# Performance work log

Hardware: AMD Instinct MI355X
Metric: run time of the kernel (lower is better)

Reference implementation:

```python
import jax, jax.numpy as jnp
import numpy as np

EPS = 1e-5
NUM_HEADS = 4
HEAD_DIM = 64
NUM_STEPS = 3


def layernorm(x, g, b):
    mu = jnp.mean(x, axis=-1, keepdims=True)
    var = jnp.mean((x - mu) ** 2, axis=-1, keepdims=True)
    return (x - mu) / jnp.sqrt(var + EPS) * g + b


def entmax15(x):
    # exact alpha=1.5 entmax along last axis (Peters et al. 2019)
    n = x.shape[-1]
    x = x - jnp.max(x, axis=-1, keepdims=True)
    x = x / 2.0
    srt = -jnp.sort(-x, axis=-1)                      # descending
    rho = jnp.arange(1, n + 1, dtype=x.dtype)
    cs = jnp.cumsum(srt, axis=-1)
    cs2 = jnp.cumsum(srt * srt, axis=-1)
    mean = cs / rho
    ss = cs2 - mean * cs                              # k * (mean_sq - mean^2)
    delta = (1.0 - ss) / rho
    d = jnp.clip(delta, 0.0)
    safe = jnp.where(d > 0, d, 1.0)
    tau = mean - jnp.where(d > 0, jnp.sqrt(safe), 0.0)
    support = (tau <= srt).astype(jnp.int32)
    k_star = jnp.sum(support, axis=-1, keepdims=True) - 1
    tau_star = jnp.take_along_axis(tau, k_star, axis=-1)
    p = jnp.clip(x - tau_star, 0.0)
    return p * p


def setup_inputs() -> dict:
    key = jax.random.key(0)
    ks = jax.random.split(key, 8)
    B, S, Dh = 2, 512, 2048
    N, Dm = 8192, 1024
    T = NUM_HEADS * HEAD_DIM  # 256
    hidden = jax.random.normal(ks[0], (B, S, Dh), dtype=jnp.float32)
    memory = jax.random.normal(ks[1], (N, Dm), dtype=jnp.float32)
    Wq = jax.random.normal(ks[2], (Dh, T), dtype=jnp.float32) * 0.02
    Wk = jax.random.normal(ks[3], (Dm, T), dtype=jnp.float32) * 0.02
    Wv = jax.random.normal(ks[4], (Dm, T), dtype=jnp.float32) * 0.02
    Wo = jax.random.normal(ks[5], (T, Dh), dtype=jnp.float32) * 0.02
    log_beta = jnp.full((NUM_HEADS,), float(np.log(1.0 / np.sqrt(HEAD_DIM))), dtype=jnp.float32)
    g_s = jnp.ones((Dh,), jnp.float32)
    b_s = jnp.zeros((Dh,), jnp.float32)
    g_m = jnp.ones((Dm,), jnp.float32)
    b_m = jnp.zeros((Dm,), jnp.float32)
    return {"hidden": hidden, "memory": memory, "Wq": Wq, "Wk": Wk, "Wv": Wv,
            "Wo": Wo, "log_beta": log_beta, "g_s": g_s, "b_s": b_s,
            "g_m": g_m, "b_m": b_m}


def reference(hidden, memory, Wq, Wk, Wv, Wo, log_beta, g_s, b_s, g_m, b_m):
    B, S, _ = hidden.shape
    N = memory.shape[0]
    H, D = NUM_HEADS, HEAD_DIM
    Q = layernorm(hidden, g_s, b_s) @ Wq                         # [B,S,H*D]
    mem_n = layernorm(memory, g_m, b_m)
    K = (mem_n @ Wk).reshape(N, H, D).transpose(1, 0, 2)         # [H,N,D]
    V = (mem_n @ Wv).reshape(N, H, D).transpose(1, 0, 2)         # [H,N,D]
    xi = Q.reshape(B, S, H, D).transpose(0, 2, 1, 3)             # [B,H,S,D]
    beta = jnp.exp(log_beta)[None, :, None, None]                # [1,H,1,1]
    for _ in range(NUM_STEPS):
        scores = jnp.einsum('bhsd,hnd->bhsn', xi, K) * beta      # [B,H,S,N]
        w = entmax15(scores)
        xi = jnp.einsum('bhsn,hnd->bhsd', w, V)
    converged = xi.transpose(0, 2, 1, 3).reshape(B, S, H * D)
    output = converged @ Wo                                      # [B,S,hidden_dim]
    return output, converged
```

## Files before the change

### kernel.cpp

```cpp
#include <hip/hip_runtime.h>
#include <math.h>

typedef _Float16 f16;
typedef f16 f16x8 __attribute__((ext_vector_type(8)));
typedef float f32x4 __attribute__((ext_vector_type(4)));

#define QSCALE 16384.0f
#define QINV 6.103515625e-5f
#define QOFF 2.5f

__device__ __forceinline__ float wred_add(float v) {
#pragma unroll
  for (int off = 32; off >= 1; off >>= 1) v += __shfl_xor(v, off, 64);
  return v;
}
__device__ __forceinline__ float wred_max(float v) {
#pragma unroll
  for (int off = 32; off >= 1; off >>= 1) v = fmaxf(v, __shfl_xor(v, off, 64));
  return v;
}

__global__ __launch_bounds__(256) void ln_stats_all_kernel(
    const float* __restrict__ hidden, const float* __restrict__ memory,
    float* __restrict__ mu_h, float* __restrict__ rs_h,
    float* __restrict__ mu_m, float* __restrict__ rs_m) {
  int b = blockIdx.x, tid = threadIdx.x;
  const float* X;
  float* mu;
  float* rs;
  int cols, row;
  if (b < 1024) { X = hidden; cols = 2048; mu = mu_h; rs = rs_h; row = b; }
  else { X = memory; cols = 1024; mu = mu_m; rs = rs_m; row = b - 1024; }
  const float4* xr = (const float4*)(X + (size_t)row * cols);
  int nv = cols >> 10;
  float s = 0.f, s2 = 0.f;
  for (int v = 0; v < nv; ++v) {
    float4 x4 = xr[tid + (v << 8)];
    s += x4.x + x4.y + x4.z + x4.w;
    s2 += x4.x * x4.x + x4.y * x4.y + x4.z * x4.z + x4.w * x4.w;
  }
  s = wred_add(s);
  s2 = wred_add(s2);
  __shared__ float rb[8];
  int wid = tid >> 6, lane = tid & 63;
  if (lane == 0) { rb[wid] = s; rb[4 + wid] = s2; }
  __syncthreads();
  if (tid == 0) {
    float S = rb[0] + rb[1] + rb[2] + rb[3];
    float S2 = rb[4] + rb[5] + rb[6] + rb[7];
    float m = S / (float)cols;
    float var = S2 / (float)cols - m * m;
    mu[row] = m;
    rs[row] = 1.f / sqrtf(var + 1e-5f);
  }
}

__global__ __launch_bounds__(256) void split_a_all_kernel(
    const float* __restrict__ hidden, const float* __restrict__ memory,
    const float* __restrict__ mu_h, const float* __restrict__ rs_h,
    const float* __restrict__ mu_m, const float* __restrict__ rs_m,
    f16x8* __restrict__ Ahh, f16x8* __restrict__ Ahl,
    f16x8* __restrict__ Amh, f16x8* __restrict__ Aml) {
  int b = blockIdx.x;
  const float* X;
  const float* mu;
  const float* rs;
  f16x8 *Ah, *Al;
  int M, Kd, b0;
  if (b < 1024) {
    X = hidden; mu = mu_h; rs = rs_h; Ah = Ahh; Al = Ahl;
    M = 1024; Kd = 2048; b0 = 0;
  } else {
    X = memory; mu = mu_m; rs = rs_m; Ah = Amh; Al = Aml;
    M = 8192; Kd = 1024; b0 = 1024;
  }
  int blk = (b - b0) * 4 + (threadIdx.x >> 6);
  int l = threadIdx.x & 63;
  int nmt = M >> 4;
  int kc = blk / nmt, mt = blk - kc * nmt;
  int m = mt * 16 + (l & 15);
  int k = kc * 32 + ((l >> 4) << 3);
  const float* src = X + (size_t)m * Kd + k;
  float mm = mu[m];
  float rr = rs[m];
  f16x8 hi, lo;
#pragma unroll
  for (int j = 0; j < 8; ++j) {
    float v = (src[j] - mm) * rr;
    f16 hv = (f16)v;
    hi[j] = hv;
    lo[j] = (f16)((v - (float)hv) * 512.f);
  }
  size_t o = ((size_t)blk << 6) + l;
  Ah[o] = hi;
  Al[o] = lo;
}

__global__ __launch_bounds__(256) void split_a_kernel(
    const float* __restrict__ X, const float* __restrict__ mu,
    const float* __restrict__ rs, f16x8* __restrict__ Ah,
    f16x8* __restrict__ Al, int M, int Kd, int lay) {
  int blk = blockIdx.x * 4 + (threadIdx.x >> 6);
  int l = threadIdx.x & 63;
  int nmt = M >> 4;
  int kc = blk / nmt, mt = blk - kc * nmt;
  int m = mt * 16 + (l & 15);
  int k = kc * 32 + ((l >> 4) << 3);
  const float* src;
  if (lay == 0) {
    src = X + (size_t)m * Kd + k;
  } else {
    int b = m >> 9, s = m & 511, hh = k >> 6, d = k & 63;
    src = X + ((((size_t)b * 4 + hh) * 512 + s) << 6) + d;
  }
  float mm = mu ? mu[m] : 0.f;
  float rr = rs ? rs[m] : 1.f;
  f16x8 hi, lo;
#pragma unroll
  for (int j = 0; j < 8; ++j) {
    float v = (src[j] - mm) * rr;
    f16 hv = (f16)v;
    hi[j] = hv;
    lo[j] = (f16)((v - (float)hv) * 512.f);
  }
  size_t o = ((size_t)blk << 6) + l;
  Ah[o] = hi;
  Al[o] = lo;
}

__global__ __launch_bounds__(256) void split_w_all_kernel(
    const float* __restrict__ Wq, const float* __restrict__ Wk,
    const float* __restrict__ Wv, const float* __restrict__ Wo,
    const float* __restrict__ g_s, const float* __restrict__ g_m,
    f16x8* __restrict__ Bqh, f16x8* __restrict__ Bql,
    f16x8* __restrict__ Bkh, f16x8* __restrict__ Bkl,
    f16x8* __restrict__ Bvh, f16x8* __restrict__ Bvl,
    f16x8* __restrict__ Boh, f16x8* __restrict__ Bol) {
  int b = blockIdx.x;
  const float* W;
  const float* g;
  f16x8 *Bh, *Bl;
  int N, base;
  if (b < 256) { W = Wq; g = g_s; Bh = Bqh; Bl = Bql; N = 256; base = 0; }
  else if (b < 384) { W = Wk; g = g_m; Bh = Bkh; Bl = Bkl; N = 256; base = 256; }
  else if (b < 512) { W = Wv; g = g_m; Bh = Bvh; Bl = Bvl; N = 256; base = 384; }
  else { W = Wo; g = nullptr; Bh = Boh; Bl = Bol; N = 2048; base = 512; }
  int blk = (b - base) * 4 + (threadIdx.x >> 6);
  int l = threadIdx.x & 63;
  int nnt = N >> 4;
  int kc = blk / nnt, nt = blk - kc * nnt;
  int n = nt * 16 + (l & 15);
  int k0 = kc * 32 + ((l >> 4) << 3);
  f16x8 hi, lo;
#pragma unroll
  for (int j = 0; j < 8; ++j) {
    float v = W[(size_t)(k0 + j) * N + n];
    if (g) v *= g[k0 + j];
    f16 hv = (f16)v;
    hi[j] = hv;
    lo[j] = (f16)((v - (float)hv) * 512.f);
  }
  size_t o = ((size_t)blk << 6) + l;
  Bh[o] = hi;
  Bl[o] = lo;
}

__global__ __launch_bounds__(256) void wcol3_kernel(
    const float* __restrict__ Wq, const float* __restrict__ bq,
    const float* __restrict__ Wk, const float* __restrict__ bk,
    const float* __restrict__ Wv, const float* __restrict__ bv,
    float* __restrict__ vbq, float* __restrict__ vbk,
    float* __restrict__ vbv) {
  int which = blockIdx.z;
  const float* W = which == 0 ? Wq : (which == 1 ? Wk : Wv);
  const float* b = which == 0 ? bq : (which == 1 ? bk : bv);
  float* vb = which == 0 ? vbq : (which == 1 ? vbk : vbv);
  int Kd = which == 0 ? 2048 : 1024;
  int t = threadIdx.x;
  int kpb = Kd >> 4;
  int k0 = blockIdx.y * kpb;
  float s = 0.f;
  for (int k = k0; k < k0 + kpb; ++k) s = fmaf(b[k], W[(size_t)k * 256 + t], s);
  atomicAdd(&vb[t], s);
}

__global__ __launch_bounds__(256) void gemm_mfma_kernel(
    const f16x8* __restrict__ Ah, const f16x8* __restrict__ Al,
    const f16x8* __restrict__ Bh, const f16x8* __restrict__ Bl,
    const float* __restrict__ vb, float* __restrict__ outf,
    f16x8* __restrict__ o16a, f16x8* __restrict__ o16b, int M, int N, int nk,
    int out_mode) {
  __shared__ __align__(16) float Ts[64][68];
  const int tid = threadIdx.x;
  const int w = tid >> 6, l = tid & 63;
  const int ql = l & 15, g = l >> 4;
  const int bn = blockIdx.x, bm = blockIdx.y;
  const size_t astr = ((size_t)(M >> 4)) << 6;
  const size_t bstr = ((size_t)(N >> 4)) << 6;
  const f16x8* aph = Ah + (((size_t)(bm * 4 + w)) << 6) + l;
  const f16x8* apl = Al + (((size_t)(bm * 4 + w)) << 6) + l;
  const f16x8* bph = Bh + (((size_t)(bn * 4)) << 6) + l;
  const f16x8* bpl = Bl + (((size_t)(bn * 4)) << 6) + l;

  f32x4 cm[4], cx[4];
#pragma unroll
  for (int nf = 0; nf < 4; ++nf) {
    cm[nf] = (f32x4){0.f, 0.f, 0.f, 0.f};
    cx[nf] = (f32x4){0.f, 0.f, 0.f, 0.f};
  }

  f16x8 a0h = aph[0], a0l = apl[0];
  f16x8 b0h[4], b0l[4];
#pragma unroll
  for (int nf = 0; nf < 4; ++nf) {
    b0h[nf] = bph[nf << 6];
    b0l[nf] = bpl[nf << 6];
  }

  for (int kc = 0; kc < nk - 1; ++kc) {
    const size_t ao = (size_t)(kc + 1) * astr;
    const size_t bo = (size_t)(kc + 1) * bstr;
    f16x8 a1h = aph[ao], a1l = apl[ao];
    f16x8 b1h[4], b1l[4];
#pragma unroll
    for (int nf = 0; nf < 4; ++nf) {
      b1h[nf] = bph[bo + (nf << 6)];
      b1l[nf] = bpl[bo + (nf << 6)];
    }
#pragma unroll
    for (int nf = 0; nf < 4; ++nf) {
      cm[nf] = __builtin_amdgcn_mfma_f32_16x16x32_f16(a0h, b0h[nf], cm[nf], 0, 0, 0);
      cx[nf] = __builtin_amdgcn_mfma_f32_16x16x32_f16(a0h, b0l[nf], cx[nf], 0, 0, 0);
      cx[nf] = __builtin_amdgcn_mfma_f32_16x16x32_f16(a0l, b0h[nf], cx[nf], 0, 0, 0);
    }
    a0h = a1h;
    a0l = a1l;
#pragma unroll
    for (int nf = 0; nf < 4; ++nf) {
      b0h[nf] = b1h[nf];
      b0l[nf] = b1l[nf];
    }
  }
#pragma unroll
  for (int nf = 0; nf < 4; ++nf) {
    cm[nf] = __builtin_amdgcn_mfma_f32_16x16x32_f16(a0h, b0h[nf], cm[nf], 0, 0, 0);
    cx[nf] = __builtin_amdgcn_mfma_f32_16x16x32_f16(a0h, b0l[nf], cx[nf], 0, 0, 0);
    cx[nf] = __builtin_amdgcn_mfma_f32_16x16x32_f16(a0l, b0h[nf], cx[nf], 0, 0, 0);
  }

  float vbc[4] = {0.f, 0.f, 0.f, 0.f};
  if (vb) {
#pragma unroll
    for (int nf = 0; nf < 4; ++nf) vbc[nf] = vb[bn * 64 + nf * 16 + ql];
  }

  if (out_mode == 0) {
#pragma unroll
    for (int nf = 0; nf < 4; ++nf)
#pragma unroll
      for (int r = 0; r < 4; ++r) {
        float val = fmaf(cx[nf][r], 0.001953125f, cm[nf][r]) + vbc[nf];
        int m = bm * 64 + w * 16 + (g << 2) + r;
        int n = bn * 64 + nf * 16 + ql;
        int b = m >> 9, s = m & 511, hh = n >> 6, d = n & 63;
        outf[((((size_t)b * 4 + hh) * 512 + s) << 6) + d] = val;
      }
  } else if (out_mode == 3) {
#pragma unroll
    for (int nf = 0; nf < 4; ++nf)
#pragma unroll
      for (int r = 0; r < 4; ++r) {
        float val = fmaf(cx[nf][r], 0.001953125f, cm[nf][r]) + vbc[nf];
        int m = bm * 64 + w * 16 + (g << 2) + r;
        int n = bn * 64 + nf * 16 + ql;
        outf[(size_t)m * N + n] = val;
      }
  } else {
#pragma unroll
    for (int nf = 0; nf < 4; ++nf)
#pragma unroll
      for (int r = 0; r < 4; ++r)
        Ts[w * 16 + (g << 2) + r][nf * 16 + ql] =
            fmaf(cx[nf][r], 0.001953125f, cm[nf][r]) + vbc[nf];
    __syncthreads();
    if (out_mode == 4) {
#pragma unroll
      for (int i = 0; i < 2; ++i) {
        int slot = tid + (i << 8);
        int blk = slot >> 6, l2 = slot & 63;
        int ktl = blk >> 1, dc = blk & 1;
        int key = (ktl << 4) + (l2 & 15);
        int db = (dc << 5) + ((l2 >> 4) << 3);
        f16x8 hi, lo;
#pragma unroll
        for (int j = 0; j < 8; ++j) {
          float v = Ts[key][db + j];
          f16 hv = (f16)v;
          hi[j] = hv;
          lo[j] = (f16)((v - (float)hv) * 512.f);
        }
        size_t o = (((size_t)(bn * 512 + bm * 4 + ktl) * 2 + dc) << 6) + l2;
        o16a[o] = hi;
        o16b[o] = lo;
      }
    } else {
#pragma unroll
      for (int i = 0; i < 2; ++i) {
        int slot = tid + (i << 8);
        int blk = slot >> 6, l2 = slot & 63;
        int dt = blk >> 1, kcl = blk & 1;
        int keyb = (kcl << 5) + ((l2 >> 4) << 3);
        int d = (dt << 4) + (l2 & 15);
        f16x8 v8;
#pragma unroll
        for (int j = 0; j < 8; ++j) v8[j] = (f16)Ts[keyb + j][d];
        size_t o = (((size_t)(bn * 4 + dt) * 256 + bm * 2 + kcl) << 6) + l2;
        o16a[o] = v8;
      }
    }
  }
}

__global__ __launch_bounds__(1024) void hop_score_kernel(
    const float* __restrict__ xi_in, const f16x8* __restrict__ Khi,
    const f16x8* __restrict__ Klo, const float* __restrict__ log_beta,
    unsigned short* __restrict__ Y) {
  __shared__ float xiq[32][64];
  __shared__ float mxb[16][32];
  __shared__ float mxs[32];
  const int tid = threadIdx.x;
  const int w = tid >> 6, l = tid & 63;
  const int ql = l & 15, g = l >> 4;
  const int bh = blockIdx.x & 7;
  const int qpair = (blockIdx.x >> 3) & 15;
  const int khalf = blockIdx.x >> 7;
  const int h = bh & 3;
  const size_t base_io = ((size_t)bh * 512 + qpair * 32) * 64;

  float beta = expf(log_beta[h]);
  for (int i = tid; i < 2048; i += 1024)
    xiq[i >> 6][i & 63] = xi_in[base_io + i] * beta;
  __syncthreads();

  f16x8 xa0, xa1, xla0, xla1;
  f16x8 xb0, xb1, xlb0, xlb1;
#pragma unroll
  for (int j = 0; j < 8; ++j) {
    float a0v = xiq[ql][(g << 3) + j];
    float a1v = xiq[ql][32 + (g << 3) + j];
    float b0v = xiq[16 + ql][(g << 3) + j];
    float b1v = xiq[16 + ql][32 + (g << 3) + j];
    f16 ha0 = (f16)a0v, ha1 = (f16)a1v, hb0 = (f16)b0v, hb1 = (f16)b1v;
    xa0[j] = ha0; xla0[j] = (f16)((a0v - (float)ha0) * 512.f);
    xa1[j] = ha1; xla1[j] = (f16)((a1v - (float)ha1) * 512.f);
    xb0[j] = hb0; xlb0[j] = (f16)((b0v - (float)hb0) * 512.f);
    xb1[j] = hb1; xlb1[j] = (f16)((b1v - (float)hb1) * 512.f);
  }

  const f16x8* kb = Khi + (size_t)h * 65536 + l;
  const f16x8* kl = Klo + (size_t)h * 65536 + l;

  {
    const int kts = w * 32;
    f16x8 sa0 = kb[(size_t)kts * 128], sa1 = kb[(size_t)kts * 128 + 64];
    f32x4 cA = {0.f, 0.f, 0.f, 0.f}, cB = {0.f, 0.f, 0.f, 0.f};
    cA = __builtin_amdgcn_mfma_f32_16x16x32_f16(sa0, xa0, cA, 0, 0, 0);
    cA = __builtin_amdgcn_mfma_f32_16x16x32_f16(sa1, xa1, cA, 0, 0, 0);
    cB = __builtin_amdgcn_mfma_f32_16x16x32_f16(sa0, xb0, cB, 0, 0, 0);
    cB = __builtin_amdgcn_mfma_f32_16x16x32_f16(sa1, xb1, cB, 0, 0, 0);
    float mA = fmaxf(fmaxf(cA[0], cA[1]), fmaxf(cA[2], cA[3]));
    float mB = fmaxf(fmaxf(cB[0], cB[1]), fmaxf(cB[2], cB[3]));
    mA = fmaxf(mA, __shfl_xor(mA, 16, 64));
    mA = fmaxf(mA, __shfl_xor(mA, 32, 64));
    mB = fmaxf(mB, __shfl_xor(mB, 16, 64));
    mB = fmaxf(mB, __shfl_xor(mB, 32, 64));
    if (l < 16) { mxb[w][ql] = mA; mxb[w][16 + ql] = mB; }
  }
  __syncthreads();
  if (tid < 32) {
    float m = mxb[0][tid];
#pragma unroll
    for (int ww = 1; ww < 16; ++ww) m = fmaxf(m, mxb[ww][tid]);
    mxs[tid] = m;
  }
  __syncthreads();
  const float qcA = QOFF * QSCALE + 0.5f - mxs[ql] * 0.5f * QSCALE;
  const float qcB = QOFF * QSCALE + 0.5f - mxs[16 + ql] * 0.5f * QSCALE;

  const size_t YbaseA = (size_t)(bh * 32 + qpair * 2) * 131072;
  const size_t YbaseB = YbaseA + 131072;
  const int kt0 = khalf * 256 + w * 16;
  for (int kt = kt0; kt < kt0 + 16; ++kt) {
    f16x8 a0 = kb[(size_t)kt * 128], a1 = kb[(size_t)kt * 128 + 64];
    f16x8 b0 = kl[(size_t)kt * 128], b1 = kl[(size_t)kt * 128 + 64];
    const size_t yoff =
        (size_t)(kt >> 1) * 512 + ql * 32 + (kt & 1) * 16 + (g << 2);
    {
      f32x4 cm = {0.f, 0.f, 0.f, 0.f}, cx = {0.f, 0.f, 0.f, 0.f};
      cm = __builtin_amdgcn_mfma_f32_16x16x32_f16(a0, xa0, cm, 0, 0, 0);
      cm = __builtin_amdgcn_mfma_f32_16x16x32_f16(a1, xa1, cm, 0, 0, 0);
      cx = __builtin_amdgcn_mfma_f32_16x16x32_f16(b0, xa0, cx, 0, 0, 0);
      cx = __builtin_amdgcn_mfma_f32_16x16x32_f16(a0, xla0, cx, 0, 0, 0);
      cx = __builtin_amdgcn_mfma_f32_16x16x32_f16(b1, xa1, cx, 0, 0, 0);
      cx = __builtin_amdgcn_mfma_f32_16x16x32_f16(a1, xla1, cx, 0, 0, 0);
      ushort4 uv;
      unsigned short* up = (unsigned short*)&uv;
#pragma unroll
      for (int r = 0; r < 4; ++r) {
        float s = fmaf(cx[r], 0.001953125f, cm[r]);
        float uq = fmaf(s, 8192.0f, qcA);
        uq = fminf(fmaxf(uq, 0.f), 65535.f);
        up[r] = (unsigned short)(int)uq;
      }
      *(ushort4*)&Y[YbaseA + yoff] = uv;
    }
    {
      f32x4 cm = {0.f, 0.f, 0.f, 0.f}, cx = {0.f, 0.f, 0.f, 0.f};
      cm = __builtin_amdgcn_mfma_f32_16x16x32_f16(a0, xb0, cm, 0, 0, 0);
      cm = __builtin_amdgcn_mfma_f32_16x16x32_f16(a1, xb1, cm, 0, 0, 0);
      cx = __builtin_amdgcn_mfma_f32_16x16x32_f16(b0, xb0, cx, 0, 0, 0);
      cx = __builtin_amdgcn_mfma_f32_16x16x32_f16(a0, xlb0, cx, 0, 0, 0);
      cx = __builtin_amdgcn_mfma_f32_16x16x32_f16(b1, xb1, cx, 0, 0, 0);
      cx = __builtin_amdgcn_mfma_f32_16x16x32_f16(a1, xlb1, cx, 0, 0, 0);
      ushort4 uv;
      unsigned short* up = (unsigned short*)&uv;
#pragma unroll
      for (int r = 0; r < 4; ++r) {
        float s = fmaf(cx[r], 0.001953125f, cm[r]);
        float uq = fmaf(s, 8192.0f, qcB);
        uq = fminf(fmaxf(uq, 0.f), 65535.f);
        up[r] = (unsigned short)(int)uq;
      }
      *(ushort4*)&Y[YbaseB + yoff] = uv;
    }
  }
}

__global__ __launch_bounds__(256) void hop_tau_kernel(
    const unsigned short* __restrict__ Y, float* __restrict__ tau) {
  const int row = blockIdx.x;
  const int bh = row >> 9, qi = row & 511;
  const int qtile = qi >> 4, ql = qi & 15;
  const size_t yb = (size_t)(bh * 32 + qtile) * 131072 + ql * 32;
  const int t = threadIdx.x;
  const uint4* p = (const uint4*)(Y + yb + (size_t)t * 512);
  float y[32];
#pragma unroll
  for (int v = 0; v < 4; ++v) {
    uint4 u = p[v];
    unsigned a[4] = {u.x, u.y, u.z, u.w};
#pragma unroll
    for (int e = 0; e < 4; ++e) {
      y[v * 8 + e * 2] = fmaf((float)(a[e] & 0xffffu), QINV, -QOFF);
      y[v * 8 + e * 2 + 1] = fmaf((float)(a[e] >> 16), QINV, -QOFF);
    }
  }
  __shared__ float redm[4];
  __shared__ float rb[5][4];
  __shared__ float rb3[3][4][3];
  const int wi = t >> 6, lane = t & 63;

  {
    float m = y[0];
#pragma unroll
    for (int i = 1; i < 32; ++i) m = fmaxf(m, y[i]);
    m = wred_max(m);
    if (lane == 0) redm[wi] = m;
  }
  __syncthreads();
  const float ymax =
      fmaxf(fmaxf(redm[0], redm[1]), fmaxf(redm[2], redm[3]));

  float lo = ymax - 1.001f, hi = ymax;
#pragma unroll 1
  for (int it = 0; it < 5; ++it) {
    float tv = 0.5f * (lo + hi);
    float f = 0.f;
#pragma unroll
    for (int i = 0; i < 32; ++i) {
      float d = fmaxf(y[i] - tv, 0.f);
      f = fmaf(d, d, f);
    }
    f = wred_add(f);
    if (lane == 0) rb[it][wi] = f;
    __syncthreads();
    float tot = rb[it][0] + rb[it][1] + rb[it][2] + rb[it][3];
    if (tot >= 1.f) lo = tv; else hi = tv;
  }

  float tc = lo;
#pragma unroll 1
  for (int it = 0; it < 3; ++it) {
    float kk = 0.f, s1 = 0.f, s2 = 0.f;
#pragma unroll
    for (int i = 0; i < 32; ++i) {
      if (y[i] > tc) { kk += 1.f; s1 += y[i]; s2 = fmaf(y[i], y[i], s2); }
    }
    kk = wred_add(kk);
    s1 = wred_add(s1);
    s2 = wred_add(s2);
    if (lane == 0) { rb3[it][wi][0] = kk; rb3[it][wi][1] = s1; rb3[it][wi][2] = s2; }
    __syncthreads();
    float K = rb3[it][0][0] + rb3[it][1][0] + rb3[it][2][0] + rb3[it][3][0];
    float S1 = rb3[it][0][1] + rb3[it][1][1] + rb3[it][2][1] + rb3[it][3][1];
    float S2 = rb3[it][0][2] + rb3[it][1][2] + rb3[it][2][2] + rb3[it][3][2];
    if (K >= 0.5f) {
      float mean = S1 / K;
      float ss = fmaf(-mean, S1, S2);
      float delta = (1.f - ss) / K;
      tc = delta > 0.f ? mean - sqrtf(delta) : mean;
    }
  }
  if (t == 0) tau[row] = tc;
}

__global__ __launch_bounds__(1024) void hop_pv_kernel(
    const unsigned short* __restrict__ Y, const f16x8* __restrict__ Vp,
    const float* __restrict__ tau, float* __restrict__ xi_out) {
  __shared__ float outp[16][16][64];
  __shared__ float taus[16];
  const int tid = threadIdx.x;
  const int w = tid >> 6, l = tid & 63;
  const int ql = l & 15, g = l >> 4;
  const int bh = blockIdx.x & 7, qtile = blockIdx.x >> 3;
  const int h = bh & 3;
  const size_t base_io = ((size_t)bh * 512 + qtile * 16) * 64;

  if (tid < 16) taus[tid] = tau[bh * 512 + qtile * 16 + tid];
  __syncthreads();
  const float t1 = taus[ql];
  const size_t Ybase = (size_t)(bh * 32 + qtile) * 131072;
  const f16x8* vb = Vp + (size_t)h * 65536 + l;

  f32x4 m2[4];
#pragma unroll
  for (int dt = 0; dt < 4; ++dt) m2[dt] = (f32x4){0.f, 0.f, 0.f, 0.f};

  for (int kc = 0; kc < 16; ++kc) {
    const int chunk = w * 16 + kc;
    uint4 uv = *(const uint4*)(Y + Ybase + (size_t)chunk * 512 + ql * 32 +
                               (g << 3));
    unsigned a[4] = {uv.x, uv.y, uv.z, uv.w};
    f16x8 a2;
#pragma unroll
    for (int e = 0; e < 4; ++e) {
      float y0 = fmaf((float)(a[e] & 0xffffu), QINV, -QOFF);
      float y1 = fmaf((float)(a[e] >> 16), QINV, -QOFF);
      float p0 = fmaxf(y0 - t1, 0.f);
      float p1 = fmaxf(y1 - t1, 0.f);
      a2[e * 2] = (f16)(p0 * p0);
      a2[e * 2 + 1] = (f16)(p1 * p1);
    }
#pragma unroll
    for (int dt = 0; dt < 4; ++dt) {
      f16x8 vf = vb[(((size_t)dt * 256 + chunk) << 6)];
      m2[dt] = __builtin_amdgcn_mfma_f32_16x16x32_f16(a2, vf, m2[dt], 0, 0, 0);
    }
  }
#pragma unroll
  for (int dt = 0; dt < 4; ++dt)
#pragma unroll
    for (int r = 0; r < 4; ++r)
      outp[w][(g << 2) + r][dt * 16 + ql] = m2[dt][r];
  __syncthreads();
  {
    float s = 0.f;
#pragma unroll
    for (int ww = 0; ww < 16; ++ww) s += outp[ww][tid >> 6][tid & 63];
    xi_out[base_io + tid] = s;
  }
}

__global__ __launch_bounds__(256) void conv_copy_kernel(
    const float* __restrict__ xi, float* __restrict__ out) {
  int o4 = blockIdx.x * 256 + threadIdx.x;
  int o = o4 << 2;
  int dd = o & 63, hq = (o >> 6) & 3, sq = (o >> 8) & 511, bq = o >> 17;
  float4 v =
      *(const float4*)&xi[((((size_t)bq << 2) + hq) * 512 + sq) * 64 + dd];
  *(float4*)&out[o] = v;
}

extern "C" void kernel_launch(void* const* d_in, const int* in_sizes, int n_in,
                              void* d_out, int out_size, void* d_ws,
                              size_t ws_size, hipStream_t stream) {
  (void)in_sizes; (void)n_in; (void)out_size; (void)ws_size;
  const float* hidden = (const float*)d_in[0];
  const float* memory = (const float*)d_in[1];
  const float* Wq = (const float*)d_in[2];
  const float* Wk = (const float*)d_in[3];
  const float* Wv = (const float*)d_in[4];
  const float* Wo = (const float*)d_in[5];
  const float* log_beta = (const float*)d_in[6];
  const float* g_s = (const float*)d_in[7];
  const float* b_s = (const float*)d_in[8];
  const float* g_m = (const float*)d_in[9];
  const float* b_m = (const float*)d_in[10];
  float* out = (float*)d_out;

  float* ws = (float*)d_ws;
  float* mu_h = ws;
  float* rs_h = ws + 1024;
  float* mu_m = ws + 2048;
  float* rs_m = ws + 10240;
  float* xiA = ws + 18432;
  float* xiB = ws + 280576;
  float* vb_q = ws + 542720;
  float* vb_k = ws + 542976;
  float* vb_v = ws + 543232;
  float* tau = ws + 543488;
  f16x8* Khi = (f16x8*)(ws + 548864);
  f16x8* Klo = Khi + 262144;
  f16x8* Vp = Klo + 262144;
  f16x8* Bqh = Vp + 262144;
  f16x8* Bql = Bqh + 65536;
  f16x8* Bkh = Bql + 65536;
  f16x8* Bkl = Bkh + 32768;
  f16x8* Bvh = Bkl + 32768;
  f16x8* Bvl = Bvh + 32768;
  f16x8* Boh = Bvl + 32768;
  f16x8* Bol = Boh + 65536;
  unsigned short* Y = (unsigned short*)(Bol + 65536);
  f16x8* Amh = (f16x8*)Y;
  f16x8* Aml = Amh + 1048576;
  f16x8* Ahh = Aml + 1048576;
  f16x8* Ahl = Ahh + 262144;
  f16x8* Axh = Ahl + 262144;
  f16x8* Axl = Axh + 32768;

  ln_stats_all_kernel<<<9216, 256, 0, stream>>>(hidden, memory, mu_h, rs_h,
                                                mu_m, rs_m);
  hipMemsetAsync(vb_q, 0, 3 * 256 * sizeof(float), stream);

  split_a_all_kernel<<<5120, 256, 0, stream>>>(hidden, memory, mu_h, rs_h,
                                               mu_m, rs_m, Ahh, Ahl, Amh, Aml);
  split_w_all_kernel<<<768, 256, 0, stream>>>(Wq, Wk, Wv, Wo, g_s, g_m, Bqh,
                                              Bql, Bkh, Bkl, Bvh, Bvl, Boh,
                                              Bol);
  wcol3_kernel<<<dim3(1, 16, 3), 256, 0, stream>>>(Wq, b_s, Wk, b_m, Wv, b_m,
                                                   vb_q, vb_k, vb_v);

  gemm_mfma_kernel<<<dim3(4, 16), 256, 0, stream>>>(
      Ahh, Ahl, Bqh, Bql, vb_q, xiA, nullptr, nullptr, 1024, 256, 64, 0);
  gemm_mfma_kernel<<<dim3(4, 128), 256, 0, stream>>>(
      Amh, Aml, Bkh, Bkl, vb_k, nullptr, Khi, Klo, 8192, 256, 32, 4);
  gemm_mfma_kernel<<<dim3(4, 128), 256, 0, stream>>>(
      Amh, Aml, Bvh, Bvl, vb_v, nullptr, Vp, nullptr, 8192, 256, 32, 5);

  float* xin = xiA;
  float* xout = xiB;
  for (int step = 0; step < 3; ++step) {
    hop_score_kernel<<<256, 1024, 0, stream>>>(xin, Khi, Klo, log_beta, Y);
    hop_tau_kernel<<<4096, 256, 0, stream>>>(Y, tau);
    hop_pv_kernel<<<256, 1024, 0, stream>>>(Y, Vp, tau, xout);
    float* t = xin; xin = xout; xout = t;
  }

  split_a_kernel<<<128, 256, 0, stream>>>(xin, nullptr, nullptr, Axh, Axl,
                                          1024, 256, 1);
  gemm_mfma_kernel<<<dim3(32, 16), 256, 0, stream>>>(
      Axh, Axl, Boh, Bol, nullptr, out, nullptr, nullptr, 1024, 2048, 8, 3);
  conv_copy_kernel<<<256, 256, 0, stream>>>(xin, out + 2097152);
}
```

Baseline: 402.2 us.

## Restructure entmax tau kernel to process a 16-row query tile per block

```diff
diff --git a/kernel.cpp b/kernel.cpp
--- a/kernel.cpp
+++ b/kernel.cpp
@@ -436,55 +436,74 @@
   }
 }
 
-__global__ __launch_bounds__(256) void hop_tau_kernel(
+__global__ __launch_bounds__(1024) void hop_tau_kernel(
     const unsigned short* __restrict__ Y, float* __restrict__ tau) {
-  const int row = blockIdx.x;
-  const int bh = row >> 9, qi = row & 511;
-  const int qtile = qi >> 4, ql = qi & 15;
-  const size_t yb = (size_t)(bh * 32 + qtile) * 131072 + ql * 32;
+  const int b = blockIdx.x;
+  const size_t sb = (size_t)b * 131072;
   const int t = threadIdx.x;
-  const uint4* p = (const uint4*)(Y + yb + (size_t)t * 512);
-  float y[32];
-#pragma unroll
-  for (int v = 0; v < 4; ++v) {
-    uint4 u = p[v];
-    unsigned a[4] = {u.x, u.y, u.z, u.w};
-#pragma unroll
-    for (int e = 0; e < 4; ++e) {
-      y[v * 8 + e * 2] = fmaf((float)(a[e] & 0xffffu), QINV, -QOFF);
-      y[v * 8 + e * 2 + 1] = fmaf((float)(a[e] >> 16), QINV, -QOFF);
-    }
-  }
-  __shared__ float redm[4];
-  __shared__ float rb[5][4];
-  __shared__ float rb3[3][4][3];
-  const int wi = t >> 6, lane = t & 63;
-
-  {
-    float m = y[0];
-#pragma unroll
-    for (int i = 1; i < 32; ++i) m = fmaxf(m, y[i]);
-    m = wred_max(m);
-    if (lane == 0) redm[wi] = m;
-  }
+  const int w = t >> 6, l = t & 63;
+  const int r = t & 15;
+
+  __shared__ float redm[16][16];
+  __shared__ float rbis[5][16][16];
+  __shared__ float rref[3][3][16][16];
+
+  const uint4* p0 = (const uint4*)(Y + sb + (size_t)t * 32);
+  const uint4* p1 = (const uint4*)(Y + sb + (size_t)t * 32 + 32768);
+  const uint4* p2 = (const uint4*)(Y + sb + (size_t)t * 32 + 65536);
+  const uint4* p3 = (const uint4*)(Y + sb + (size_t)t * 32 + 98304);
+  uint4 q0 = p0[0], q1 = p0[1], q2 = p0[2], q3 = p0[3];
+  uint4 q4 = p1[0], q5 = p1[1], q6 = p1[2], q7 = p1[3];
+  uint4 q8 = p2[0], q9 = p2[1], q10 = p2[2], q11 = p2[3];
+  uint4 q12 = p3[0], q13 = p3[1], q14 = p3[2], q15 = p3[3];
+
+#define EACH_DW(OP)                                                          \
+  OP(q0.x) OP(q0.y) OP(q0.z) OP(q0.w) OP(q1.x) OP(q1.y) OP(q1.z) OP(q1.w)    \
+  OP(q2.x) OP(q2.y) OP(q2.z) OP(q2.w) OP(q3.x) OP(q3.y) OP(q3.z) OP(q3.w)    \
+  OP(q4.x) OP(q4.y) OP(q4.z) OP(q4.w) OP(q5.x) OP(q5.y) OP(q5.z) OP(q5.w)    \
+  OP(q6.x) OP(q6.y) OP(q6.z) OP(q6.w) OP(q7.x) OP(q7.y) OP(q7.z) OP(q7.w)    \
+  OP(q8.x) OP(q8.y) OP(q8.z) OP(q8.w) OP(q9.x) OP(q9.y) OP(q9.z) OP(q9.w)    \
+  OP(q10.x) OP(q10.y) OP(q10.z) OP(q10.w)                                    \
+  OP(q11.x) OP(q11.y) OP(q11.z) OP(q11.w)                                    \
+  OP(q12.x) OP(q12.y) OP(q12.z) OP(q12.w)                                    \
+  OP(q13.x) OP(q13.y) OP(q13.z) OP(q13.w)                                    \
+  OP(q14.x) OP(q14.y) OP(q14.z) OP(q14.w)                                    \
+  OP(q15.x) OP(q15.y) OP(q15.z) OP(q15.w)
+
+  unsigned um = 0;
+#define OPMX(u) { unsigned a = (u) & 0xffffu, bb = (u) >> 16;                \
+                  if (a > um) um = a; if (bb > um) um = bb; }
+  EACH_DW(OPMX)
+#undef OPMX
+  float my = (float)um;
+  my = fmaxf(my, __shfl_xor(my, 16, 64));
+  my = fmaxf(my, __shfl_xor(my, 32, 64));
+  if (l < 16) redm[w][l] = my;
   __syncthreads();
-  const float ymax =
-      fmaxf(fmaxf(redm[0], redm[1]), fmaxf(redm[2], redm[3]));
+  float umaxf = redm[0][r];
+#pragma unroll
+  for (int ww = 1; ww < 16; ++ww) umaxf = fmaxf(umaxf, redm[ww][r]);
+  const float ymax = fmaf(umaxf, QINV, -QOFF);
 
   float lo = ymax - 1.001f, hi = ymax;
 #pragma unroll 1
   for (int it = 0; it < 5; ++it) {
     float tv = 0.5f * (lo + hi);
     float f = 0.f;
-#pragma unroll
-    for (int i = 0; i < 32; ++i) {
-      float d = fmaxf(y[i] - tv, 0.f);
-      f = fmaf(d, d, f);
-    }
-    f = wred_add(f);
-    if (lane == 0) rb[it][wi] = f;
+#define OPBI(u) { float y0 = fmaf((float)((u) & 0xffffu), QINV, -QOFF);      \
+                  float y1 = fmaf((float)((u) >> 16), QINV, -QOFF);          \
+                  float d0 = fmaxf(y0 - tv, 0.f);                            \
+                  float d1 = fmaxf(y1 - tv, 0.f);                            \
+                  f = fmaf(d0, d0, f); f = fmaf(d1, d1, f); }
+    EACH_DW(OPBI)
+#undef OPBI
+    f += __shfl_xor(f, 16, 64);
+    f += __shfl_xor(f, 32, 64);
+    if (l < 16) rbis[it][w][l] = f;
     __syncthreads();
-    float tot = rb[it][0] + rb[it][1] + rb[it][2] + rb[it][3];
+    float tot = 0.f;
+#pragma unroll
+    for (int ww = 0; ww < 16; ++ww) tot += rbis[it][ww][r];
     if (tot >= 1.f) lo = tv; else hi = tv;
   }
 
@@ -492,18 +511,31 @@
 #pragma unroll 1
   for (int it = 0; it < 3; ++it) {
     float kk = 0.f, s1 = 0.f, s2 = 0.f;
-#pragma unroll
-    for (int i = 0; i < 32; ++i) {
-      if (y[i] > tc) { kk += 1.f; s1 += y[i]; s2 = fmaf(y[i], y[i], s2); }
-    }
-    kk = wred_add(kk);
-    s1 = wred_add(s1);
-    s2 = wred_add(s2);
-    if (lane == 0) { rb3[it][wi][0] = kk; rb3[it][wi][1] = s1; rb3[it][wi][2] = s2; }
+#define OPRF(u) { float y0 = fmaf((float)((u) & 0xffffu), QINV, -QOFF);      \
+                  float y1 = fmaf((float)((u) >> 16), QINV, -QOFF);          \
+                  if (y0 > tc) { kk += 1.f; s1 += y0; s2 = fmaf(y0, y0, s2); } \
+                  if (y1 > tc) { kk += 1.f; s1 += y1; s2 = fmaf(y1, y1, s2); } }
+    EACH_DW(OPRF)
+#undef OPRF
+    kk += __shfl_xor(kk, 16, 64);
+    kk += __shfl_xor(kk, 32, 64);
+    s1 += __shfl_xor(s1, 16, 64);
+    s1 += __shfl_xor(s1, 32, 64);
+    s2 += __shfl_xor(s2, 16, 64);
+    s2 += __shfl_xor(s2, 32, 64);
+    if (l < 16) {
+      rref[it][0][w][l] = kk;
+      rref[it][1][w][l] = s1;
+      rref[it][2][w][l] = s2;
+    }
     __syncthreads();
-    float K = rb3[it][0][0] + rb3[it][1][0] + rb3[it][2][0] + rb3[it][3][0];
-    float S1 = rb3[it][0][1] + rb3[it][1][1] + rb3[it][2][1] + rb3[it][3][1];
-    float S2 = rb3[it][0][2] + rb3[it][1][2] + rb3[it][2][2] + rb3[it][3][2];
+    float K = 0.f, S1 = 0.f, S2 = 0.f;
+#pragma unroll
+    for (int ww = 0; ww < 16; ++ww) {
+      K += rref[it][0][ww][r];
+      S1 += rref[it][1][ww][r];
+      S2 += rref[it][2][ww][r];
+    }
     if (K >= 0.5f) {
       float mean = S1 / K;
       float ss = fmaf(-mean, S1, S2);
@@ -511,7 +543,11 @@
       tc = delta > 0.f ? mean - sqrtf(delta) : mean;
     }
   }
-  if (t == 0) tau[row] = tc;
+#undef EACH_DW
+  if (t < 16) {
+    const int bh = b >> 5, qtile = b & 31;
+    tau[bh * 512 + qtile * 16 + t] = tc;
+  }
 }
 
 __global__ __launch_bounds__(1024) void hop_pv_kernel(
@@ -651,7 +687,7 @@
   float* xout = xiB;
   for (int step = 0; step < 3; ++step) {
     hop_score_kernel<<<256, 1024, 0, stream>>>(xin, Khi, Klo, log_beta, Y);
-    hop_tau_kernel<<<4096, 256, 0, stream>>>(Y, tau);
+    hop_tau_kernel<<<256, 1024, 0, stream>>>(Y, tau);
     hop_pv_kernel<<<256, 1024, 0, stream>>>(Y, Vp, tau, xout);
     float* t = xin; xin = xout; xout = t;
   }
```

New measurement: 532.1 us. 1.32x slower.
